# Performance work log

Measured on AMD Instinct MI355X. Metric: run time of the kernel, lower is better.

The kernel has to match this reference:

```python
import jax, jax.numpy as jnp
import numpy as np


def setup_inputs() -> dict:
    key = jax.random.key(0)
    kx, ky = jax.random.split(key)
    B, N, M, D = 4, 4096, 4096, 128
    xd = jax.random.normal(kx, (B, N, D), dtype=jnp.float32)
    yd = jax.random.normal(ky, (B, M, D), dtype=jnp.float32)
    mask = jnp.ones((B, N, M), dtype=jnp.float32)
    return {"xd": xd, "yd": yd, "mask": mask}


def _pairwise_l2(x, y):
    # x: (B, N, D), y: (B, M, D) -> (B, N, M) euclidean distances
    x2 = jnp.sum(x * x, axis=-1)[:, :, None]          # (B, N, 1)
    y2 = jnp.sum(y * y, axis=-1)[:, None, :]          # (B, 1, M)
    xy = jnp.einsum("bnd,bmd->bnm", x, y)             # (B, N, M)
    d2 = jnp.maximum(x2 + y2 - 2.0 * xy, 0.0)
    return jnp.sqrt(d2)


def reference(xd, yd, mask):
    # NNDFMatcher.forward: orientation='x', smallest=True, topk=None
    dists = _pairwise_l2(xd, yd) * mask               # (B, N, M)
    pairs = jnp.argmin(dists, axis=-1)                # (B, N) int
    top_dists = jnp.min(dists, axis=-1)               # (B, N)
    M = mask.shape[-1]
    # one-hot scatter: match_mask[b, n, pairs[b, n]] = 1
    match_mask = (pairs[..., None] == jnp.arange(M)[None, None, :]).astype(mask.dtype)
    return match_mask, pairs, top_dists
```

## Files before the change

### kernel.cpp

```cpp
#include <hip/hip_runtime.h>


typedef float  f32x4   __attribute__((ext_vector_type(4)));
typedef float  f32x16  __attribute__((ext_vector_type(16)));
typedef short  bf16x8  __attribute__((ext_vector_type(8)));

#define PS ((size_t)2097152)

#define WAITVM_(N) asm volatile("s_waitcnt vmcnt(" #N ")" ::: "memory")
#define WAITVM(N)  WAITVM_(N)
#define BAR        __builtin_amdgcn_s_barrier()
#define FENCE      asm volatile("" ::: "memory")

__device__ __forceinline__ unsigned short f2bf(float x) {
    unsigned u = __float_as_uint(x);
    u += 0x7FFFu + ((u >> 16) & 1u);
    return (unsigned short)(u >> 16);
}
__device__ __forceinline__ float bf2f(unsigned short s) {
    return __uint_as_float(((unsigned)s) << 16);
}
__device__ __forceinline__ void gload_lds16(const void* g, void* l) {
    __builtin_amdgcn_global_load_lds(
        (const __attribute__((address_space(1))) void*)g,
        (__attribute__((address_space(3))) void*)l, 16, 0, 0);
}

__global__ __launch_bounds__(256) void k_prep(const float* __restrict__ xd,
                                              const float* __restrict__ yd,
                                              unsigned short* __restrict__ pl,
                                              float* __restrict__ ws) {
    __shared__ float sm[4][16];
    int bid  = blockIdx.x;
    int i    = bid >> 10;
    int b    = (bid >> 8) & 3;
    int rblk = bid & 255;
    int tid  = threadIdx.x;
    int kb   = tid >> 6;
    int l    = tid & 63;
    int lg4  = (l >> 4) & 3;
    int r    = rblk * 16 + (l & 15);
    int k0   = kb * 32 + lg4 * 8;
    const float* src = (i ? yd : xd) + ((size_t)(b * 4096 + r) * 128 + k0);
    float v[8];
    *reinterpret_cast<float4*>(v)     = *reinterpret_cast<const float4*>(src);
    *reinterpret_cast<float4*>(v + 4) = *reinterpret_cast<const float4*>(src + 4);
    bf16x8 hv, mv, lv;
    float s = 0.f;
    #pragma unroll
    for (int e = 0; e < 8; ++e) {
        float x = v[e];
        s = fmaf(x, x, s);
        unsigned short h  = f2bf(x);
        float r1 = x - bf2f(h);
        unsigned short m  = f2bf(r1);
        float r2 = r1 - bf2f(m);
        unsigned short lo = f2bf(r2);
        hv[e] = (short)h; mv[e] = (short)m; lv[e] = (short)lo;
    }
    int kh   = kb >> 1;
    int kc2  = (kb & 1) * 2 + (lg4 >> 1);
    int land = (r & 31) + ((lg4 & 1) << 5);
    size_t base = ((size_t)((b * 2 + kh) * 128 + (rblk >> 1))) * 2048
                + (size_t)(kc2 * 64 + land) * 8;
    unsigned short* dst = pl + (size_t)(i * 3) * PS;
    *reinterpret_cast<bf16x8*>(dst + base)          = hv;
    *reinterpret_cast<bf16x8*>(dst + base + PS)     = mv;
    *reinterpret_cast<bf16x8*>(dst + base + 2 * PS) = lv;
    s += __shfl_xor(s, 16);
    s += __shfl_xor(s, 32);
    if (l < 16) sm[kb][l] = s;
    __syncthreads();
    if (tid < 16) {
        float t = sm[0][tid] + sm[1][tid] + sm[2][tid] + sm[3][tid];
        ws[(i ? 16384 : 0) + b * 4096 + rblk * 16 + tid] = t;
    }
}

__global__ __launch_bounds__(512, 1) void k_gemm(const float* __restrict__ mask,
                                                 const float* __restrict__ ws,
                                                 const unsigned short* __restrict__ pl,
                                                 float* __restrict__ out,
                                                 float* __restrict__ pv,
                                                 int* __restrict__ pi) {
    __shared__ __align__(16) unsigned short Ab[2][2][8192];
    __shared__ __align__(16) unsigned short Bp[2][3][8192];

    const int bid = blockIdx.x;
    const int xcd = bid & 7;
    const int b   = xcd >> 1;
    const int ch  = xcd & 1;
    const int rt  = bid >> 3;
    const int tid = threadIdx.x;
    const int w   = tid >> 6, l = tid & 63;
    const int wr  = w >> 1, wc = w & 1;
    const int l31 = l & 31, lg1 = l >> 5;
    const int g0  = b * 4096 + rt * 128;

    float x2r[16];
    #pragma unroll
    for (int rg = 0; rg < 16; ++rg)
        x2r[rg] = ws[g0 + wr * 32 + (rg & 3) + 8 * (rg >> 2) + 4 * lg1];

    const float* y2g = ws + 16384 + b * 4096 + ch * 2048 + wc * 64 + l31;

    #pragma unroll
    for (int kh = 0; kh < 2; ++kh)
        #pragma unroll
        for (int ap = 0; ap < 2; ++ap) {
            const unsigned short* Ac = pl + (size_t)ap * PS
                + (((size_t)((b * 2 + kh) * 128 + rt * 4)) << 11);
            gload_lds16((const char*)Ac + w * 1024 + l * 16,
                        (char*)(&Ab[kh][ap][0]) + w * 1024);
            gload_lds16((const char*)Ac + 8192 + w * 1024 + l * 16,
                        (char*)(&Ab[kh][ap][0]) + 8192 + w * 1024);
        }
    bf16x8 Al[2][4];
    #pragma unroll
    for (int kh = 0; kh < 2; ++kh)
        #pragma unroll
        for (int kc = 0; kc < 4; ++kc)
            Al[kh][kc] = *reinterpret_cast<const bf16x8*>(
                pl + (size_t)2 * PS
                + (((size_t)((b * 2 + kh) * 128 + rt * 4 + wr)) << 11)
                + (size_t)(kc * 64 + l) * 8);

#define STAGE_B(NTT, KH, SLOT) do {                                               \
    _Pragma("unroll") for (int bp_ = 0; bp_ < 3; ++bp_) {                         \
        const unsigned short* Bc_ = pl + (size_t)(3 + bp_) * PS                   \
            + (((size_t)((b * 2 + (KH)) * 128 + ch * 64 + (NTT) * 4)) << 11);     \
        gload_lds16((const char*)Bc_ + w * 1024 + l * 16,                         \
                    (char*)(&Bp[SLOT][bp_][0]) + w * 1024);                       \
        gload_lds16((const char*)Bc_ + 8192 + w * 1024 + l * 16,                  \
                    (char*)(&Bp[SLOT][bp_][0]) + 8192 + w * 1024);                \
    }                                                                             \
} while (0)

#define MLOAD34(NT) do {                                                          \
    _Pragma("unroll") for (int K = 0; K < 32; ++K) {                              \
        const int rg_ = K >> 1, ni_ = K & 1;                                      \
        const int row_ = wr * 32 + (rg_ & 3) + 8 * (rg_ >> 2) + 4 * lg1;          \
        pm[K] = mask[(size_t)(g0 + row_) * 4096                                   \
                     + (ch * 2048 + (NT) * 128 + wc * 64 + ni_ * 32 + l31)];      \
    }                                                                             \
    yv[0] = y2g[(NT) * 128];                                                      \
    yv[1] = y2g[(NT) * 128 + 32];                                                 \
} while (0)

#define ZST(NT, I) do {                                                           \
    const f32x4 z_ = (f32x4){0.f, 0.f, 0.f, 0.f};                                 \
    const int r_ = (tid >> 5) * 8 + (I);                                          \
    *reinterpret_cast<f32x4*>(out + (size_t)(g0 + r_) * 4096                      \
        + ch * 2048 + (NT) * 128 + ((tid & 31) << 2)) = z_;                       \
} while (0)

#define COMPUTE(KH, SLOT) do {                                                    \
    __builtin_amdgcn_s_setprio(1);                                                \
    _Pragma("unroll") for (int kc = 0; kc < 4; ++kc) {                            \
        const int fa = (((wr * 4 + kc) * 64) + l) * 8;                            \
        bf16x8 Ah_ = *reinterpret_cast<const bf16x8*>(&Ab[KH][0][fa]);            \
        bf16x8 Am_ = *reinterpret_cast<const bf16x8*>(&Ab[KH][1][fa]);            \
        bf16x8 Al_ = Al[KH][kc];                                                  \
        _Pragma("unroll") for (int ni = 0; ni < 2; ++ni) {                        \
            const int fb = ((((wc * 2 + ni) * 4 + kc) * 64) + l) * 8;             \
            bf16x8 Bh_ = *reinterpret_cast<const bf16x8*>(&Bp[SLOT][0][fb]);      \
            bf16x8 Bm_ = *reinterpret_cast<const bf16x8*>(&Bp[SLOT][1][fb]);      \
            bf16x8 Bl_ = *reinterpret_cast<const bf16x8*>(&Bp[SLOT][2][fb]);      \
            f32x16 c_ = acc[ni];                                                  \
            c_ = __builtin_amdgcn_mfma_f32_32x32x16_bf16(Ah_, Bh_, c_, 0, 0, 0);  \
            c_ = __builtin_amdgcn_mfma_f32_32x32x16_bf16(Am_, Bh_, c_, 0, 0, 0);  \
            c_ = __builtin_amdgcn_mfma_f32_32x32x16_bf16(Al_, Bh_, c_, 0, 0, 0);  \
            c_ = __builtin_amdgcn_mfma_f32_32x32x16_bf16(Ah_, Bm_, c_, 0, 0, 0);  \
            c_ = __builtin_amdgcn_mfma_f32_32x32x16_bf16(Am_, Bm_, c_, 0, 0, 0);  \
            c_ = __builtin_amdgcn_mfma_f32_32x32x16_bf16(Ah_, Bl_, c_, 0, 0, 0);  \
            acc[ni] = c_;                                                         \
        }                                                                         \
    }                                                                             \
    __builtin_amdgcn_s_setprio(0);                                                \
} while (0)

    float pm[32], yv[2];
    f32x16 acc[2];

    STAGE_B(0, 0, 0);
    MLOAD34(0);
    WAITVM(0);
    BAR;

    const double INITD = __hiloint2double(0x7f7fffff, 0);
    double bv[16];
    #pragma unroll
    for (int q = 0; q < 16; ++q) bv[q] = INITD;

    #pragma unroll 1
    for (int nt = 0; nt < 16; ++nt) {
        const int ntn = (nt < 15) ? nt + 1 : 15;

        WAITVM(4); BAR;
        #pragma unroll
        for (int ni = 0; ni < 2; ++ni)
            #pragma unroll
            for (int e = 0; e < 16; ++e) acc[ni][e] = 0.f;
        STAGE_B(nt, 1, 1);
        FENCE;
        if (nt > 0) MLOAD34(nt);
        ZST(nt, 0); ZST(nt, 1); ZST(nt, 2); ZST(nt, 3);
        COMPUTE(0, 0);

        WAITVM(38); BAR;
        STAGE_B(ntn, 0, 0);
        FENCE;
        ZST(nt, 4); ZST(nt, 5); ZST(nt, 6); ZST(nt, 7);
        COMPUTE(1, 1);

        #pragma unroll
        for (int ni = 0; ni < 2; ++ni) {
            const int c = ch * 2048 + nt * 128 + wc * 64 + ni * 32 + l31;
            #pragma unroll
            for (int rg = 0; rg < 16; ++rg) {
                float d2 = fmaf(acc[ni][rg], -2.0f, x2r[rg]) + yv[ni];
                float d  = sqrtf(fmaxf(d2, 0.0f)) * pm[rg * 2 + ni];
                double pk = __hiloint2double(__float_as_int(d), c);
                bv[rg] = fmin(bv[rg], pk);
            }
        }
    }
#undef STAGE_B
#undef MLOAD34
#undef ZST
#undef COMPUTE

    WAITVM(0);

    #pragma unroll
    for (int off = 1; off < 32; off <<= 1) {
        #pragma unroll
        for (int q = 0; q < 16; ++q)
            bv[q] = fmin(bv[q], __shfl_xor(bv[q], off));
    }
    __syncthreads();
    double* cd = reinterpret_cast<double*>(&Bp[0][0][0]);
    if (l31 == 0) {
        #pragma unroll
        for (int rg = 0; rg < 16; ++rg) {
            int rowl = wr * 32 + (rg & 3) + 8 * (rg >> 2) + 4 * lg1;
            cd[rowl * 2 + wc] = bv[rg];
        }
    }
    __syncthreads();
    if (tid < 128) {
        double v = fmin(cd[tid * 2], cd[tid * 2 + 1]);
        int grow = g0 + tid;
        pv[grow * 2 + ch] = __int_as_float(__double2hiint(v));
        pi[grow * 2 + ch] = __double2loint(v);
    }
}

__global__ __launch_bounds__(256) void k_fin(const float* __restrict__ pv,
                                             const int* __restrict__ pi,
                                             float* __restrict__ out) {
    int t = blockIdx.x * 256 + threadIdx.x;
    float v0 = pv[t * 2], v1 = pv[t * 2 + 1];
    int   i0 = pi[t * 2], i1 = pi[t * 2 + 1];
    bool take1 = (v1 < v0) || (v1 == v0 && i1 < i0);
    float v  = take1 ? v1 : v0;
    int   ix = take1 ? i1 : i0;
    out[67108864 + t]         = (float)ix;
    out[67108864 + 16384 + t] = v;
    out[(size_t)t * 4096 + (size_t)ix] = 1.0f;
}

__global__ __launch_bounds__(256) void k_rowsq(const float* __restrict__ xd,
                                               const float* __restrict__ yd,
                                               float* __restrict__ ws) {
    int tid  = threadIdx.x;
    int wid  = tid >> 6, lane = tid & 63;
    int gr   = blockIdx.x * 4 + wid;
    const float* src = (gr < 16384) ? (xd + (size_t)gr * 128)
                                    : (yd + (size_t)(gr - 16384) * 128);
    float2 v = reinterpret_cast<const float2*>(src)[lane];
    float s  = v.x * v.x + v.y * v.y;
    for (int off = 32; off > 0; off >>= 1) s += __shfl_down(s, off);
    if (lane == 0) ws[gr] = s;
}

__global__ __launch_bounds__(256, 1) void k_main_fb(const float* __restrict__ xd,
                                                    const float* __restrict__ yd,
                                                    const float* __restrict__ mask,
                                                    const float* __restrict__ ws,
                                                    float* __restrict__ pvals,
                                                    int* __restrict__ pidx,
                                                    float* __restrict__ mm) {
    __shared__ __align__(16) float Xs[128 * 128];
    __shared__ __align__(16) float Ys[128 * 128];
    const int bid  = blockIdx.x;
    const int mh   = bid & 1;
    const int rb   = (bid >> 1) & 31;
    const int b    = bid >> 6;
    const int tid  = threadIdx.x;
    const int ty   = tid >> 4;
    const int tx   = tid & 15;
    const int row0 = rb * 128;
    const int m0   = mh * 2048;
    {
        const float4 z = make_float4(0.f, 0.f, 0.f, 0.f);
        size_t base = ((size_t)(b * 4096 + row0)) * 4096 + (size_t)m0;
        for (int r = 0; r < 128; ++r) {
            float4* p = reinterpret_cast<float4*>(mm + base + (size_t)r * 4096);
            p[tid] = z; p[tid + 256] = z;
        }
    }
    {
        int lrow = tid >> 5, slot = tid & 31;
        for (int p = 0; p < 16; ++p) {
            int row  = p * 8 + lrow;
            float4 v = reinterpret_cast<const float4*>(
                           xd + ((size_t)(b * 4096 + row0 + row)) * 128)[slot];
            int ss = slot ^ (row & 31);
            *reinterpret_cast<float4*>(&Xs[row * 128 + (ss << 2)]) = v;
        }
    }
    float x2r[8];
    #pragma unroll
    for (int i = 0; i < 8; ++i) x2r[i] = ws[b * 4096 + row0 + ty * 8 + i];
    const float* y2g = ws + 16384 + b * 4096;
    float bv[8]; int bi[8];
    #pragma unroll
    for (int i = 0; i < 8; ++i) { bv[i] = 3.4e38f; bi[i] = 0; }
    __syncthreads();
    for (int tile = 0; tile < 16; ++tile) {
        const int mbase = m0 + tile * 128;
        {
            int lrow = tid >> 5, slot = tid & 31;
            for (int p = 0; p < 16; ++p) {
                int row  = p * 8 + lrow;
                float4 v = reinterpret_cast<const float4*>(
                               yd + ((size_t)(b * 4096 + mbase + row)) * 128)[slot];
                int ss = slot ^ (row & 31);
                *reinterpret_cast<float4*>(&Ys[row * 128 + (ss << 2)]) = v;
            }
        }
        __syncthreads();
        float acc[8][8];
        #pragma unroll
        for (int i = 0; i < 8; ++i)
            #pragma unroll
            for (int jj = 0; jj < 8; ++jj) acc[i][jj] = 0.0f;
        #pragma unroll 4
        for (int ks = 0; ks < 32; ++ks) {
            float4 bf[8];
            #pragma unroll
            for (int jj = 0; jj < 8; ++jj) {
                int c = jj * 16 + tx;
                bf[jj] = *reinterpret_cast<const float4*>(&Ys[c * 128 + ((ks ^ (c & 31)) << 2)]);
            }
            #pragma unroll
            for (int i = 0; i < 8; ++i) {
                int r = ty * 8 + i;
                float4 a = *reinterpret_cast<const float4*>(&Xs[r * 128 + ((ks ^ (r & 31)) << 2)]);
                #pragma unroll
                for (int jj = 0; jj < 8; ++jj) {
                    acc[i][jj] = fmaf(a.x, bf[jj].x, acc[i][jj]);
                    acc[i][jj] = fmaf(a.y, bf[jj].y, acc[i][jj]);
                    acc[i][jj] = fmaf(a.z, bf[jj].z, acc[i][jj]);
                    acc[i][jj] = fmaf(a.w, bf[jj].w, acc[i][jj]);
                }
            }
        }
        float y2v[8];
        #pragma unroll
        for (int jj = 0; jj < 8; ++jj) y2v[jj] = y2g[mbase + jj * 16 + tx];
        #pragma unroll
        for (int i = 0; i < 8; ++i) {
            int r = ty * 8 + i;
            const float* mr = mask + ((size_t)(b * 4096 + row0 + r)) * 4096;
            #pragma unroll
            for (int jj = 0; jj < 8; ++jj) {
                int   m  = mbase + jj * 16 + tx;
                float d2 = x2r[i] + y2v[jj] - 2.0f * acc[i][jj];
                float d  = sqrtf(fmaxf(d2, 0.0f)) * mr[m];
                if (d < bv[i]) { bv[i] = d; bi[i] = m; }
            }
        }
        __syncthreads();
    }
    float* candv = Xs;
    int*   candi = reinterpret_cast<int*>(Xs + 2048);
    #pragma unroll
    for (int i = 0; i < 8; ++i) {
        int r = ty * 8 + i;
        candv[r * 16 + tx] = bv[i];
        candi[r * 16 + tx] = bi[i];
    }
    __syncthreads();
    if (tid < 128) {
        int   r  = tid;
        float v  = candv[r * 16];
        int   ix = candi[r * 16];
        for (int t = 1; t < 16; ++t) {
            float v2 = candv[r * 16 + t];
            int   i2 = candi[r * 16 + t];
            if (v2 < v || (v2 == v && i2 < ix)) { v = v2; ix = i2; }
        }
        int grow = b * 4096 + row0 + r;
        pvals[grow * 2 + mh] = v;
        pidx [grow * 2 + mh] = ix;
    }
}

__global__ __launch_bounds__(256) void k_fin_fb(const float* __restrict__ pvals,
                                                const int* __restrict__ pidx,
                                                float* __restrict__ out) {
    int t = blockIdx.x * 256 + threadIdx.x;
    float v0 = pvals[t * 2], v1 = pvals[t * 2 + 1];
    int   i0 = pidx [t * 2], i1 = pidx [t * 2 + 1];
    bool take1 = (v1 < v0) || (v1 == v0 && i1 < i0);
    float v  = take1 ? v1 : v0;
    int   ix = take1 ? i1 : i0;
    out[67108864 + t]         = (float)ix;
    out[67108864 + 16384 + t] = v;
    out[(size_t)t * 4096 + (size_t)ix] = 1.0f;
}

extern "C" void kernel_launch(void* const* d_in, const int* in_sizes, int n_in,
                              void* d_out, int out_size, void* d_ws, size_t ws_size,
                              hipStream_t stream) {
    const float* xd   = (const float*)d_in[0];
    const float* yd   = (const float*)d_in[1];
    const float* mask = (const float*)d_in[2];
    float* out = (float*)d_out;
    float* wsf = (float*)d_ws;

    const size_t need = 131072 + 6 * PS * 2 + 262144;
    if (ws_size >= need) {
        unsigned short* pl = (unsigned short*)((char*)d_ws + 131072);
        float* pv = (float*)((char*)d_ws + 131072 + 6 * PS * 2);
        int*   pi = (int*)  ((char*)d_ws + 131072 + 6 * PS * 2 + 131072);
        k_prep <<<2048, 256, 0, stream>>>(xd, yd, pl, wsf);
        k_gemm <<<256,  512, 0, stream>>>(mask, wsf, pl, out, pv, pi);
        k_fin  <<<64,   256, 0, stream>>>(pv, pi, out);
    } else {
        float* pvals = wsf + 32768;
        int*   pidx  = (int*)(wsf + 65536);
        k_rowsq  <<<8192, 256, 0, stream>>>(xd, yd, wsf);
        k_main_fb<<<256,  256, 0, stream>>>(xd, yd, mask, wsf, pvals, pidx, out);
        k_fin_fb <<<64,   256, 0, stream>>>(pvals, pidx, out);
    }
}
```

Before: 184.8 us.

## Halve GEMM block tile to 64x64 with 256 threads, two blocks per CU

Restructures k_gemm from 512-thread blocks with 128x128 tiles into 256-thread blocks with 64x64 tiles. The grid doubles to 512 blocks, launch bounds allow two blocks per CU, and LDS buffers, mask prefetch, zero stores and the MFMA loop shrink to one accumulator per wave. The goal is better occupancy and latency hiding across blocks. The cost is more B-operand reloads per output element, since each tile is reused less, plus more loop iterations and barriers.

```diff
diff --git a/kernel.cpp b/kernel.cpp
--- a/kernel.cpp
+++ b/kernel.cpp
@@ -77,14 +77,14 @@
     }
 }
 
-__global__ __launch_bounds__(512, 1) void k_gemm(const float* __restrict__ mask,
+__global__ __launch_bounds__(256, 2) void k_gemm(const float* __restrict__ mask,
                                                  const float* __restrict__ ws,
                                                  const unsigned short* __restrict__ pl,
                                                  float* __restrict__ out,
                                                  float* __restrict__ pv,
                                                  int* __restrict__ pi) {
-    __shared__ __align__(16) unsigned short Ab[2][2][8192];
-    __shared__ __align__(16) unsigned short Bp[2][3][8192];
+    __shared__ __align__(16) unsigned short Ab[2][2][4096];
+    __shared__ __align__(16) unsigned short Bp[2][3][4096];
 
     const int bid = blockIdx.x;
     const int xcd = bid & 7;
@@ -95,95 +95,87 @@
     const int w   = tid >> 6, l = tid & 63;
     const int wr  = w >> 1, wc = w & 1;
     const int l31 = l & 31, lg1 = l >> 5;
-    const int g0  = b * 4096 + rt * 128;
+    const int g0  = b * 4096 + rt * 64;
 
     float x2r[16];
     #pragma unroll
     for (int rg = 0; rg < 16; ++rg)
         x2r[rg] = ws[g0 + wr * 32 + (rg & 3) + 8 * (rg >> 2) + 4 * lg1];
 
-    const float* y2g = ws + 16384 + b * 4096 + ch * 2048 + wc * 64 + l31;
+    const float* y2g = ws + 16384 + b * 4096 + ch * 2048 + wc * 32 + l31;
 
     #pragma unroll
     for (int kh = 0; kh < 2; ++kh)
         #pragma unroll
         for (int ap = 0; ap < 2; ++ap) {
             const unsigned short* Ac = pl + (size_t)ap * PS
-                + (((size_t)((b * 2 + kh) * 128 + rt * 4)) << 11);
-            gload_lds16((const char*)Ac + w * 1024 + l * 16,
-                        (char*)(&Ab[kh][ap][0]) + w * 1024);
-            gload_lds16((const char*)Ac + 8192 + w * 1024 + l * 16,
-                        (char*)(&Ab[kh][ap][0]) + 8192 + w * 1024);
+                + (((size_t)((b * 2 + kh) * 128 + rt * 2)) << 11);
+            gload_lds16((const char*)Ac + tid * 16,
+                        (char*)(&Ab[kh][ap][0]) + tid * 16);
+            gload_lds16((const char*)Ac + 4096 + tid * 16,
+                        (char*)(&Ab[kh][ap][0]) + 4096 + tid * 16);
         }
     bf16x8 Al[2][4];
     #pragma unroll
-    for (int kh = 0; kh < 2; ++kh)
+    for (int kh = 0; kh < 2; ++kh) {
+        const unsigned short* Ac = pl + (size_t)2 * PS
+            + (((size_t)((b * 2 + kh) * 128 + rt * 2 + wr)) << 11);
         #pragma unroll
         for (int kc = 0; kc < 4; ++kc)
-            Al[kh][kc] = *reinterpret_cast<const bf16x8*>(
-                pl + (size_t)2 * PS
-                + (((size_t)((b * 2 + kh) * 128 + rt * 4 + wr)) << 11)
-                + (size_t)(kc * 64 + l) * 8);
-
-#define STAGE_B(NTT, KH, SLOT) do {                                               \
+            Al[kh][kc] = *reinterpret_cast<const bf16x8*>(Ac + (kc * 64 + l) * 8);
+    }
+
+#define STAGE_B(CT, KH, SLOT) do {                                                \
     _Pragma("unroll") for (int bp_ = 0; bp_ < 3; ++bp_) {                         \
         const unsigned short* Bc_ = pl + (size_t)(3 + bp_) * PS                   \
-            + (((size_t)((b * 2 + (KH)) * 128 + ch * 64 + (NTT) * 4)) << 11);     \
-        gload_lds16((const char*)Bc_ + w * 1024 + l * 16,                         \
-                    (char*)(&Bp[SLOT][bp_][0]) + w * 1024);                       \
-        gload_lds16((const char*)Bc_ + 8192 + w * 1024 + l * 16,                  \
-                    (char*)(&Bp[SLOT][bp_][0]) + 8192 + w * 1024);                \
+            + (((size_t)((b * 2 + (KH)) * 128 + ch * 64 + (CT) * 2)) << 11);      \
+        gload_lds16((const char*)Bc_ + tid * 16,                                  \
+                    (char*)(&Bp[SLOT][bp_][0]) + tid * 16);                       \
+        gload_lds16((const char*)Bc_ + 4096 + tid * 16,                           \
+                    (char*)(&Bp[SLOT][bp_][0]) + 4096 + tid * 16);                \
     }                                                                             \
 } while (0)
 
-#define MLOAD34(NT) do {                                                          \
-    _Pragma("unroll") for (int K = 0; K < 32; ++K) {                              \
-        const int rg_ = K >> 1, ni_ = K & 1;                                      \
-        const int row_ = wr * 32 + (rg_ & 3) + 8 * (rg_ >> 2) + 4 * lg1;          \
+#define MLOAD16(CT) do {                                                          \
+    _Pragma("unroll") for (int K = 0; K < 16; ++K) {                              \
+        const int row_ = wr * 32 + (K & 3) + 8 * (K >> 2) + 4 * lg1;              \
         pm[K] = mask[(size_t)(g0 + row_) * 4096                                   \
-                     + (ch * 2048 + (NT) * 128 + wc * 64 + ni_ * 32 + l31)];      \
+                     + (ch * 2048 + (CT) * 64 + wc * 32 + l31)];                  \
     }                                                                             \
-    yv[0] = y2g[(NT) * 128];                                                      \
-    yv[1] = y2g[(NT) * 128 + 32];                                                 \
+    yv = y2g[(CT) * 64];                                                          \
 } while (0)
 
-#define ZST(NT, I) do {                                                           \
+#define ZST(CT, I) do {                                                           \
     const f32x4 z_ = (f32x4){0.f, 0.f, 0.f, 0.f};                                 \
-    const int r_ = (tid >> 5) * 8 + (I);                                          \
-    *reinterpret_cast<f32x4*>(out + (size_t)(g0 + r_) * 4096                      \
-        + ch * 2048 + (NT) * 128 + ((tid & 31) << 2)) = z_;                       \
+    *reinterpret_cast<f32x4*>(out + (size_t)(g0 + (I) * 16 + (tid >> 4)) * 4096   \
+        + ch * 2048 + (CT) * 64 + ((tid & 15) << 2)) = z_;                        \
 } while (0)
 
 #define COMPUTE(KH, SLOT) do {                                                    \
     __builtin_amdgcn_s_setprio(1);                                                \
     _Pragma("unroll") for (int kc = 0; kc < 4; ++kc) {                            \
-        const int fa = (((wr * 4 + kc) * 64) + l) * 8;                            \
+        const int fa = wr * 2048 + kc * 512 + l * 8;                              \
         bf16x8 Ah_ = *reinterpret_cast<const bf16x8*>(&Ab[KH][0][fa]);            \
         bf16x8 Am_ = *reinterpret_cast<const bf16x8*>(&Ab[KH][1][fa]);            \
         bf16x8 Al_ = Al[KH][kc];                                                  \
-        _Pragma("unroll") for (int ni = 0; ni < 2; ++ni) {                        \
-            const int fb = ((((wc * 2 + ni) * 4 + kc) * 64) + l) * 8;             \
-            bf16x8 Bh_ = *reinterpret_cast<const bf16x8*>(&Bp[SLOT][0][fb]);      \
-            bf16x8 Bm_ = *reinterpret_cast<const bf16x8*>(&Bp[SLOT][1][fb]);      \
-            bf16x8 Bl_ = *reinterpret_cast<const bf16x8*>(&Bp[SLOT][2][fb]);      \
-            f32x16 c_ = acc[ni];                                                  \
-            c_ = __builtin_amdgcn_mfma_f32_32x32x16_bf16(Ah_, Bh_, c_, 0, 0, 0);  \
-            c_ = __builtin_amdgcn_mfma_f32_32x32x16_bf16(Am_, Bh_, c_, 0, 0, 0);  \
-            c_ = __builtin_amdgcn_mfma_f32_32x32x16_bf16(Al_, Bh_, c_, 0, 0, 0);  \
-            c_ = __builtin_amdgcn_mfma_f32_32x32x16_bf16(Ah_, Bm_, c_, 0, 0, 0);  \
-            c_ = __builtin_amdgcn_mfma_f32_32x32x16_bf16(Am_, Bm_, c_, 0, 0, 0);  \
-            c_ = __builtin_amdgcn_mfma_f32_32x32x16_bf16(Ah_, Bl_, c_, 0, 0, 0);  \
-            acc[ni] = c_;                                                         \
-        }                                                                         \
+        const int fb = wc * 2048 + kc * 512 + l * 8;                              \
+        bf16x8 Bh_ = *reinterpret_cast<const bf16x8*>(&Bp[SLOT][0][fb]);          \
+        bf16x8 Bm_ = *reinterpret_cast<const bf16x8*>(&Bp[SLOT][1][fb]);          \
+        bf16x8 Bl_ = *reinterpret_cast<const bf16x8*>(&Bp[SLOT][2][fb]);          \
+        acc = __builtin_amdgcn_mfma_f32_32x32x16_bf16(Ah_, Bh_, acc, 0, 0, 0);    \
+        acc = __builtin_amdgcn_mfma_f32_32x32x16_bf16(Am_, Bh_, acc, 0, 0, 0);    \
+        acc = __builtin_amdgcn_mfma_f32_32x32x16_bf16(Al_, Bh_, acc, 0, 0, 0);    \
+        acc = __builtin_amdgcn_mfma_f32_32x32x16_bf16(Ah_, Bm_, acc, 0, 0, 0);    \
+        acc = __builtin_amdgcn_mfma_f32_32x32x16_bf16(Am_, Bm_, acc, 0, 0, 0);    \
+        acc = __builtin_amdgcn_mfma_f32_32x32x16_bf16(Ah_, Bl_, acc, 0, 0, 0);    \
     }                                                                             \
     __builtin_amdgcn_s_setprio(0);                                                \
 } while (0)
 
-    float pm[32], yv[2];
-    f32x16 acc[2];
+    float pm[16], yv;
+    f32x16 acc;
 
     STAGE_B(0, 0, 0);
-    MLOAD34(0);
     WAITVM(0);
     BAR;
 
@@ -193,40 +185,38 @@
     for (int q = 0; q < 16; ++q) bv[q] = INITD;
 
     #pragma unroll 1
-    for (int nt = 0; nt < 16; ++nt) {
-        const int ntn = (nt < 15) ? nt + 1 : 15;
-
-        WAITVM(4); BAR;
-        #pragma unroll
-        for (int ni = 0; ni < 2; ++ni)
-            #pragma unroll
-            for (int e = 0; e < 16; ++e) acc[ni][e] = 0.f;
-        STAGE_B(nt, 1, 1);
+    for (int ct = 0; ct < 32; ++ct) {
+        const int ctn = (ct < 31) ? ct + 1 : 31;
+
+        WAITVM(2); BAR;
+        #pragma unroll
+        for (int e = 0; e < 16; ++e) acc[e] = 0.f;
+        STAGE_B(ct, 1, 1);
         FENCE;
-        if (nt > 0) MLOAD34(nt);
-        ZST(nt, 0); ZST(nt, 1); ZST(nt, 2); ZST(nt, 3);
+        MLOAD16(ct);
+        FENCE;
+        ZST(ct, 0); ZST(ct, 1);
         COMPUTE(0, 0);
 
-        WAITVM(38); BAR;
-        STAGE_B(ntn, 0, 0);
+        WAITVM(18); BAR;
+        STAGE_B(ctn, 0, 0);
         FENCE;
-        ZST(nt, 4); ZST(nt, 5); ZST(nt, 6); ZST(nt, 7);
+        ZST(ct, 2); ZST(ct, 3);
         COMPUTE(1, 1);
 
-        #pragma unroll
-        for (int ni = 0; ni < 2; ++ni) {
-            const int c = ch * 2048 + nt * 128 + wc * 64 + ni * 32 + l31;
+        {
+            const int c = ch * 2048 + ct * 64 + wc * 32 + l31;
             #pragma unroll
             for (int rg = 0; rg < 16; ++rg) {
-                float d2 = fmaf(acc[ni][rg], -2.0f, x2r[rg]) + yv[ni];
-                float d  = sqrtf(fmaxf(d2, 0.0f)) * pm[rg * 2 + ni];
+                float d2 = fmaf(acc[rg], -2.0f, x2r[rg]) + yv;
+                float d  = sqrtf(fmaxf(d2, 0.0f)) * pm[rg];
                 double pk = __hiloint2double(__float_as_int(d), c);
                 bv[rg] = fmin(bv[rg], pk);
             }
         }
     }
 #undef STAGE_B
-#undef MLOAD34
+#undef MLOAD16
 #undef ZST
 #undef COMPUTE
 
@@ -248,7 +238,7 @@
         }
     }
     __syncthreads();
-    if (tid < 128) {
+    if (tid < 64) {
         double v = fmin(cd[tid * 2], cd[tid * 2 + 1]);
         int grow = g0 + tid;
         pv[grow * 2 + ch] = __int_as_float(__double2hiint(v));
@@ -437,7 +427,7 @@
         float* pv = (float*)((char*)d_ws + 131072 + 6 * PS * 2);
         int*   pi = (int*)  ((char*)d_ws + 131072 + 6 * PS * 2 + 131072);
         k_prep <<<2048, 256, 0, stream>>>(xd, yd, pl, wsf);
-        k_gemm <<<256,  512, 0, stream>>>(mask, wsf, pl, out, pv, pi);
+        k_gemm <<<512,  256, 0, stream>>>(mask, wsf, pl, out, pv, pi);
         k_fin  <<<64,   256, 0, stream>>>(pv, pi, out);
     } else {
         float* pvals = wsf + 32768;
```

Measured after the change: 179.0 us. 3.2% less time.
